# Kernel tuning notes

Measured on AMD Instinct MI355X. Metric: run time of the kernel, lower is better.

## Reference

```python
import jax, jax.numpy as jnp
import numpy as np

B, S, D, H = 8, 1300, 1080, 12
DK = D // H  # 90
FF = 3 * D   # 3240
EPS = 1e-5


def _layernorm(x, g, b):
    m = jnp.mean(x, axis=-1, keepdims=True)
    v = jnp.var(x, axis=-1, keepdims=True)
    return (x - m) * jax.lax.rsqrt(v + EPS) * g + b


def _rotate_half(x):
    x1, x2 = jnp.split(x, 2, axis=-1)
    return jnp.concatenate([-x2, x1], axis=-1)


def _rope(x, cos, sin):
    # x: [B,H,S,DK]; cos/sin: [S,DK] broadcast over batch/heads
    return x * cos + _rotate_half(x) * sin


def setup_inputs() -> dict:
    key = jax.random.key(0)
    ks = jax.random.split(key, 20)
    w = lambda k, sh: jax.random.normal(k, sh, dtype=jnp.float32) * 0.02
    inp = {
        'x': jax.random.normal(ks[0], (B, S, D), dtype=jnp.float32),
        'mask': jnp.tril(jnp.ones((S, S), dtype=jnp.int32))[None, None, :, :],
        'Wq': w(ks[1], (D, D)), 'bq': jnp.zeros((D,), jnp.float32),
        'Wk': w(ks[2], (D, D)), 'bk': jnp.zeros((D,), jnp.float32),
        'Wv': w(ks[3], (D, D)), 'bv': jnp.zeros((D,), jnp.float32),
        'Wo': w(ks[4], (D, D)), 'bo': jnp.zeros((D,), jnp.float32),
        'W1': w(ks[5], (D, FF)), 'b1': jnp.zeros((FF,), jnp.float32),
        'W2': w(ks[6], (FF, D)), 'b2': jnp.zeros((D,), jnp.float32),
        'W3': w(ks[7], (D, FF)), 'b3': jnp.zeros((FF,), jnp.float32),
        'ln1_g': jnp.ones((D,), jnp.float32), 'ln1_b': jnp.zeros((D,), jnp.float32),
        'ln2_g': jnp.ones((D,), jnp.float32), 'ln2_b': jnp.zeros((D,), jnp.float32),
    }
    # RoPE tables (buffers, not trainable)
    inv_freq = 1.0 / (10000.0 ** (jnp.arange(0, DK, 2, dtype=jnp.float32) / DK))
    t = jnp.arange(S, dtype=jnp.float32)
    freqs = t[:, None] * inv_freq[None, :]          # [S, DK/2]
    emb = jnp.concatenate([freqs, freqs], axis=-1)  # [S, DK]
    inp['rope_cos'] = jnp.cos(emb)
    inp['rope_sin'] = jnp.sin(emb)
    return inp


def reference(x, mask, Wq, bq, Wk, bk, Wv, bv, Wo, bo,
              W1, b1, W2, b2, W3, b3, ln1_g, ln1_b, ln2_g, ln2_b,
              rope_cos, rope_sin):
    # pre-norm attention block
    x2 = _layernorm(x, ln1_g, ln1_b)
    q = (x2 @ Wq + bq).reshape(B, S, H, DK).transpose(0, 2, 1, 3)  # [B,H,S,DK]
    k = (x2 @ Wk + bk).reshape(B, S, H, DK).transpose(0, 2, 1, 3)
    v = (x2 @ Wv + bv).reshape(B, S, H, DK).transpose(0, 2, 1, 3)
    q = _rope(q, rope_cos, rope_sin)
    k = _rope(k, rope_cos, rope_sin)
    scores = jnp.einsum('bhqd,bhkd->bhqk', q, k) / jnp.sqrt(jnp.float32(DK))
    scores = jnp.where(mask == 0, jnp.float32(-1e9), scores)
    p = jax.nn.softmax(scores, axis=-1)
    attn = jnp.einsum('bhqk,bhkd->bhqd', p, v)
    attn = attn.transpose(0, 2, 1, 3).reshape(B, S, D)
    x = x + (attn @ Wo + bo)
    # pre-norm SwiGLU FFN block
    x2 = _layernorm(x, ln2_g, ln2_b)
    h = jax.nn.silu(x2 @ W1 + b1) * (x2 @ W3 + b3)
    x = x + (h @ W2 + b2)
    return x
```

## Files before the change

### kernel.cpp

```cpp
#include <hip/hip_runtime.h>
#include <hip/hip_bf16.h>
#include <cstdint>
#include <cstddef>

#define B_  8
#define S_  1300
#define D_  1080
#define H_  12
#define DK_ 90
#define FF_ 3240
#define MROWS (B_*S_)
#define KP1 1088
#define KP2 3264
#define SP  1312
#define QKVN 3240
#define QSCALE 0.105409255338946f

typedef __hip_bfloat16 bf16;
typedef __bf16 bf16x8 __attribute__((ext_vector_type(8)));
typedef float  f32x4  __attribute__((ext_vector_type(4)));
typedef unsigned short u16x8 __attribute__((ext_vector_type(8)));

__device__ __forceinline__ void gload16(const void* g, void* l) {
    __builtin_amdgcn_global_load_lds((const __attribute__((address_space(1))) void*)g,
                                     (__attribute__((address_space(3))) void*)l, 16, 0, 0);
}
__device__ __forceinline__ unsigned short bf16bits(float f) {
    bf16 b = __float2bfloat16(f);
    return *(unsigned short*)&b;
}

__global__ __launch_bounds__(256) void zero_pads(bf16* __restrict__ buf)
{
    const int idx = blockIdx.x * 256 + threadIdx.x;
    if (idx >= MROWS * (KP1 - D_)) return;
    const int row = idx >> 3, col = D_ + (idx & 7);
    buf[(size_t)row * KP1 + col] = __float2bfloat16(0.f);
}

__global__ __launch_bounds__(256) void bcat(const float* __restrict__ bq,
    const float* __restrict__ bk, const float* __restrict__ bv,
    float* __restrict__ bqkv)
{
    const int i = blockIdx.x * 256 + threadIdx.x;
    if (i >= QKVN) return;
    bqkv[i] = (i < D_) ? bq[i] : (i < 2 * D_) ? bk[i - D_] : bv[i - 2 * D_];
}

__global__ __launch_bounds__(256) void castT(const float* __restrict__ W,
    bf16* __restrict__ WT, int K, int N, int KP)
{
    __shared__ unsigned short t[32][33];
    const int tx = threadIdx.x & 31, ty = threadIdx.x >> 5;
    const int k0 = blockIdx.x * 32, n0 = blockIdx.y * 32;
    #pragma unroll
    for (int i = 0; i < 4; ++i) {
        const int k = k0 + ty + 8 * i;
        const int n = n0 + tx;
        float v = (k < K && n < N) ? W[(size_t)k * N + n] : 0.f;
        t[ty + 8 * i][tx] = bf16bits(v);
    }
    __syncthreads();
    #pragma unroll
    for (int i = 0; i < 4; ++i) {
        const int n = n0 + ty + 8 * i;
        const int kk = k0 + tx;
        if (n < N && kk < KP) *(unsigned short*)&WT[(size_t)n * KP + kk] = t[tx][ty + 8 * i];
    }
}

__global__ __launch_bounds__(256) void ln_kernel(const float* __restrict__ x,
    const float* __restrict__ g, const float* __restrict__ b,
    bf16* __restrict__ y)
{
    __shared__ float xs[D_];
    __shared__ float red[8];
    const int row = blockIdx.x;
    const int tid = threadIdx.x;
    const float* xr = x + (size_t)row * D_;

    float s = 0.f, sq = 0.f;
    for (int d = tid; d < D_; d += 256) {
        float v = xr[d];
        xs[d] = v;
        s += v; sq += v * v;
    }
    #pragma unroll
    for (int off = 32; off > 0; off >>= 1) {
        s  += __shfl_down(s,  off, 64);
        sq += __shfl_down(sq, off, 64);
    }
    const int wave = tid >> 6, lane = tid & 63;
    if (lane == 0) { red[wave] = s; red[4 + wave] = sq; }
    __syncthreads();
    if (tid == 0) {
        float ts = 0.f, tq = 0.f;
        #pragma unroll
        for (int w = 0; w < 4; ++w) { ts += red[w]; tq += red[4 + w]; }
        red[0] = ts; red[4] = tq;
    }
    __syncthreads();
    const float mean = red[0] * (1.0f / D_);
    const float var  = red[4] * (1.0f / D_) - mean * mean;
    const float rstd = rsqrtf(var + 1e-5f);
    bf16* yr = y + (size_t)row * KP1;
    for (int d = tid; d < D_; d += 256)
        yr[d] = __float2bfloat16((xs[d] - mean) * rstd * g[d] + b[d]);
}

template<int MODE>
__global__ __launch_bounds__(256) void gemm_bf16(
    const bf16* __restrict__ A, const bf16* __restrict__ BT,
    const float* __restrict__ bias, const float* __restrict__ res,
    float* __restrict__ Cf, bf16* __restrict__ Cb,
    int M, int N, int KP, int LDC, int NP)
{
    __shared__ unsigned short As[128 * 32];
    __shared__ unsigned short Bs[128 * 32];

    const int tid = threadIdx.x;
    const int w = tid >> 6, l = tid & 63;
    const int m0 = blockIdx.y * 128, n0 = blockIdx.x * 128;

    const int rs = w * 16 + (l >> 2);
    const int kc = (l & 3) * 8;
    const int ar0 = min(m0 + rs,      M - 1);
    const int ar1 = min(m0 + rs + 64, M - 1);
    const int br0 = min(n0 + rs,      N - 1);
    const int br1 = min(n0 + rs + 64, N - 1);

    const int wm = (w >> 1) * 64, wn = (w & 1) * 64;
    const int lr = l & 15, kq = l >> 4;

    const unsigned short* aptr[4];
    const unsigned short* bptr[4];
    #pragma unroll
    for (int i = 0; i < 4; ++i) {
        aptr[i] = &As[(wm + i * 16 + lr) * 32 + kq * 8];
        bptr[i] = &Bs[(wn + i * 16 + lr) * 32 + kq * 8];
    }

    f32x4 acc[4][4] = {};

    const int nkt = KP >> 5;
    for (int kt = 0; kt < nkt; ++kt) {
        const int k0 = kt << 5;
        __syncthreads();
        gload16(A  + (size_t)ar0 * KP + k0 + kc, &As[w * 512]);
        gload16(A  + (size_t)ar1 * KP + k0 + kc, &As[2048 + w * 512]);
        gload16(BT + (size_t)br0 * KP + k0 + kc, &Bs[w * 512]);
        gload16(BT + (size_t)br1 * KP + k0 + kc, &Bs[2048 + w * 512]);
        __syncthreads();

        bf16x8 af[4], bv[4];
        #pragma unroll
        for (int i = 0; i < 4; ++i) af[i] = *(const bf16x8*)aptr[i];
        #pragma unroll
        for (int j = 0; j < 4; ++j) bv[j] = *(const bf16x8*)bptr[j];
        #pragma unroll
        for (int i = 0; i < 4; ++i)
            #pragma unroll
            for (int j = 0; j < 4; ++j)
                acc[i][j] = __builtin_amdgcn_mfma_f32_16x16x32_bf16(af[i], bv[j], acc[i][j], 0, 0, 0);
    }

    #pragma unroll
    for (int j = 0; j < 4; ++j) {
        const int n = n0 + wn + j * 16 + lr;
        if (n >= NP) continue;
        const bool real = (n < N);
        const float bn = real ? bias[n] : 0.f;
        #pragma unroll
        for (int i = 0; i < 4; ++i) {
            const int rowb = m0 + wm + i * 16 + kq * 4;
            #pragma unroll
            for (int r = 0; r < 4; ++r) {
                const int m = rowb + r;
                if (m < M) {
                    const size_t off = (size_t)m * LDC + n;
                    float val = acc[i][j][r] + bn;
                    if (MODE == 0) Cf[off] = val;
                    if (MODE == 1) Cf[off] = val + res[off];
                    if (MODE == 3) Cb[off] = real ? __float2bfloat16(val) : __float2bfloat16(0.f);
                    if (MODE == 2) {
                        if (real) {
                            const float prev = __bfloat162float(Cb[off]);
                            const float sig  = 1.0f / (1.0f + __expf(-prev));
                            Cb[off] = __float2bfloat16(prev * sig * val);
                        } else {
                            Cb[off] = __float2bfloat16(0.f);
                        }
                    }
                }
            }
        }
    }
}

__global__ __launch_bounds__(256) void rope_qk(const bf16* __restrict__ qkv,
    const float* __restrict__ cosb, const float* __restrict__ sinb,
    bf16* __restrict__ Qa, bf16* __restrict__ Ka)
{
    const int s = blockIdx.x;
    const int b = blockIdx.y;
    const int tid = threadIdx.x;

    if (s >= S_) {
        for (int idx = tid; idx < H_ * 96; idx += 256) {
            const int h = idx / 96, c = idx - (idx / 96) * 96;
            const size_t o = ((size_t)(b * H_ + h) * SP + s) * 96 + c;
            Qa[o] = __float2bfloat16(0.f);
            Ka[o] = __float2bfloat16(0.f);
        }
        return;
    }

    const bf16* row = qkv + (size_t)(b * S_ + s) * QKVN;

    for (int idx = tid; idx < H_ * 45; idx += 256) {
        const int h = idx / 45, d = idx - (idx / 45) * 45;
        const float c1 = cosb[s * DK_ + d],      s1 = sinb[s * DK_ + d];
        const float c2 = cosb[s * DK_ + d + 45], s2 = sinb[s * DK_ + d + 45];
        const size_t o = ((size_t)(b * H_ + h) * SP + s) * 96;
        const float q1 = __bfloat162float(row[h * DK_ + d]);
        const float q2 = __bfloat162float(row[h * DK_ + d + 45]);
        Qa[o + d]      = __float2bfloat16((q1 * c1 - q2 * s1) * QSCALE);
        Qa[o + d + 45] = __float2bfloat16((q2 * c2 + q1 * s2) * QSCALE);
        const float k1 = __bfloat162float(row[D_ + h * DK_ + d]);
        const float k2 = __bfloat162float(row[D_ + h * DK_ + d + 45]);
        Ka[o + d]      = __float2bfloat16(k1 * c1 - k2 * s1);
        Ka[o + d + 45] = __float2bfloat16(k2 * c2 + k1 * s2);
    }
    for (int idx = tid; idx < H_ * 6; idx += 256) {
        const int h = idx / 6, c = 90 + (idx - (idx / 6) * 6);
        const size_t o = ((size_t)(b * H_ + h) * SP + s) * 96 + c;
        Qa[o] = __float2bfloat16(0.f);
        Ka[o] = __float2bfloat16(0.f);
    }
}

__global__ __launch_bounds__(256) void vtrans(const bf16* __restrict__ qkv,
    bf16* __restrict__ Vt)
{
    __shared__ float T[96][33];
    const int k0 = blockIdx.x * 32;
    const int bh = blockIdx.y;
    const int b = bh / H_, h = bh % H_;
    const int tid = threadIdx.x;

    for (int idx = tid; idx < 32 * 90; idx += 256) {
        const int r = idx / 90, d = idx - (idx / 90) * 90;
        const int s = k0 + r;
        T[d][r] = (s < S_) ?
            __bfloat162float(qkv[(size_t)(b * S_ + s) * QKVN + 2 * D_ + h * DK_ + d]) : 0.f;
    }
    for (int idx = tid; idx < 32 * 6; idx += 256) {
        const int r = idx / 6, d = 90 + (idx - (idx / 6) * 6);
        T[d][r] = 0.f;
    }
    __syncthreads();
    for (int idx = tid; idx < 96 * 4; idx += 256) {
        const int d = idx >> 2, kk = (idx & 3) * 8;
        u16x8 v;
        #pragma unroll
        for (int i = 0; i < 8; ++i) v[i] = bf16bits(T[d][kk + i]);
        *(u16x8*)(Vt + ((size_t)bh * 96 + d) * SP + k0 + kk) = v;
    }
}

__global__ __launch_bounds__(256) void attn_mfma(const bf16* __restrict__ Qa,
    const bf16* __restrict__ Ka, const bf16* __restrict__ Vt,
    bf16* __restrict__ ab)
{
    __shared__ unsigned short Qs[64][104];
    __shared__ unsigned short Ks[32][104];
    __shared__ unsigned short Vs[96][40];
    __shared__ unsigned short Ps[4][16][40];

    const int tid = threadIdx.x;
    const int w = tid >> 6, l = tid & 63;
    const int lr = l & 15, kq = l >> 4;
    const int qblk = (int)gridDim.x - 1 - (int)blockIdx.x;
    const int q0 = qblk * 64;
    const int bh = blockIdx.y;
    const int b = bh / H_, h = bh % H_;

    const bf16* Qg = Qa + (size_t)bh * SP * 96;
    const bf16* Kg = Ka + (size_t)bh * SP * 96;
    const bf16* Vg = Vt + (size_t)bh * 96 * SP;

    for (int c = tid; c < 768; c += 256) {
        const int row = c / 12, cc = c - row * 12;
        const int rg = q0 + row;
        u16x8 v = (u16x8)0;
        if (rg < SP) v = *(const u16x8*)(Qg + (size_t)rg * 96 + cc * 8);
        *(u16x8*)&Qs[row][cc * 8] = v;
    }
    __syncthreads();

    bf16x8 Qf[3];
    #pragma unroll
    for (int kf = 0; kf < 3; ++kf)
        Qf[kf] = *(const bf16x8*)&Qs[w * 16 + lr][kf * 32 + kq * 8];

    const int qw0 = q0 + w * 16;
    const int myq = qw0 + lr;
    const int wlq = (qw0 < S_) ? min(qw0 + 15, S_ - 1) : -1;
    const int lastq = min(q0 + 63, S_ - 1);
    const int ntiles = lastq / 32 + 1;

    f32x4 Of[6] = {};
    float mrun = -1e30f, lrun = 0.f;

    for (int kt = 0; kt < ntiles; ++kt) {
        const int k0 = kt * 32;
        __syncthreads();
        for (int c = tid; c < 384; c += 256) {
            const int row = c / 12, cc = c - (c / 12) * 12;
            *(u16x8*)&Ks[row][cc * 8] = *(const u16x8*)(Kg + (size_t)(k0 + row) * 96 + cc * 8);
        }
        for (int c = tid; c < 384; c += 256) {
            const int d = c >> 2, kk = (c & 3) * 8;
            *(u16x8*)&Vs[d][kk] = *(const u16x8*)(Vg + (size_t)d * SP + k0 + kk);
        }
        __syncthreads();

        if (k0 > wlq) continue;

        f32x4 sg0 = {0.f, 0.f, 0.f, 0.f}, sg1 = {0.f, 0.f, 0.f, 0.f};
        #pragma unroll
        for (int kf = 0; kf < 3; ++kf) {
            bf16x8 k0f = *(const bf16x8*)&Ks[lr][kf * 32 + kq * 8];
            bf16x8 k1f = *(const bf16x8*)&Ks[16 + lr][kf * 32 + kq * 8];
            sg0 = __builtin_amdgcn_mfma_f32_16x16x32_bf16(k0f, Qf[kf], sg0, 0, 0, 0);
            sg1 = __builtin_amdgcn_mfma_f32_16x16x32_bf16(k1f, Qf[kf], sg1, 0, 0, 0);
        }

        float e[8];
        float msub = -1e30f;
        #pragma unroll
        for (int r = 0; r < 4; ++r) {
            const int ka = k0 + 4 * kq + r;
            const int kb = ka + 16;
            const float a = (ka <= myq && ka < S_) ? sg0[r] : -1e30f;
            const float c = (kb <= myq && kb < S_) ? sg1[r] : -1e30f;
            e[r] = a; e[4 + r] = c;
            msub = fmaxf(msub, fmaxf(a, c));
        }
        msub = fmaxf(msub, __shfl_xor(msub, 16, 64));
        msub = fmaxf(msub, __shfl_xor(msub, 32, 64));
        const float nm = fmaxf(mrun, msub);
        const float resc = __expf(mrun - nm);
        mrun = nm;
        float ls = 0.f;
        #pragma unroll
        for (int i = 0; i < 8; ++i) {
            const float ev = (e[i] > -1e29f) ? __expf(e[i] - nm) : 0.f;
            e[i] = ev; ls += ev;
        }
        ls += __shfl_xor(ls, 16, 64);
        ls += __shfl_xor(ls, 32, 64);
        lrun = lrun * resc + ls;

        ushort4 p0, p1;
        p0.x = bf16bits(e[0]); p0.y = bf16bits(e[1]); p0.z = bf16bits(e[2]); p0.w = bf16bits(e[3]);
        p1.x = bf16bits(e[4]); p1.y = bf16bits(e[5]); p1.z = bf16bits(e[6]); p1.w = bf16bits(e[7]);
        *(ushort4*)&Ps[w][lr][4 * kq]      = p0;
        *(ushort4*)&Ps[w][lr][16 + 4 * kq] = p1;

        float rf[4];
        #pragma unroll
        for (int r = 0; r < 4; ++r) rf[r] = __shfl(resc, 4 * kq + r, 16);
        #pragma unroll
        for (int c = 0; c < 6; ++c)
            #pragma unroll
            for (int r = 0; r < 4; ++r)
                Of[c][r] *= rf[r];

        bf16x8 Pf = *(const bf16x8*)&Ps[w][lr][kq * 8];
        #pragma unroll
        for (int c = 0; c < 6; ++c) {
            bf16x8 Vf = *(const bf16x8*)&Vs[16 * c + lr][kq * 8];
            Of[c] = __builtin_amdgcn_mfma_f32_16x16x32_bf16(Pf, Vf, Of[c], 0, 0, 0);
        }
    }

    const float invq = 1.0f / lrun;
    float inv[4];
    #pragma unroll
    for (int r = 0; r < 4; ++r) inv[r] = __shfl(invq, 4 * kq + r, 16);
    #pragma unroll
    for (int c = 0; c < 6; ++c) {
        const int dim = 16 * c + lr;
        if (dim >= DK_) continue;
        #pragma unroll
        for (int r = 0; r < 4; ++r) {
            const int qrow = qw0 + 4 * kq + r;
            if (qrow < S_)
                ab[(size_t)(b * S_ + qrow) * KP1 + h * DK_ + dim] =
                    __float2bfloat16(Of[c][r] * inv[r]);
        }
    }
}

extern "C" void kernel_launch(void* const* d_in, const int* in_sizes, int n_in,
                              void* d_out, int out_size, void* d_ws, size_t ws_size,
                              hipStream_t stream)
{
    const float* x    = (const float*)d_in[0];
    const float* Wq   = (const float*)d_in[2];
    const float* bq   = (const float*)d_in[3];
    const float* Wk   = (const float*)d_in[4];
    const float* bk   = (const float*)d_in[5];
    const float* Wv   = (const float*)d_in[6];
    const float* bv   = (const float*)d_in[7];
    const float* Wo   = (const float*)d_in[8];
    const float* bo   = (const float*)d_in[9];
    const float* W1   = (const float*)d_in[10];
    const float* b1   = (const float*)d_in[11];
    const float* W2   = (const float*)d_in[12];
    const float* b2   = (const float*)d_in[13];
    const float* W3   = (const float*)d_in[14];
    const float* b3   = (const float*)d_in[15];
    const float* ln1g = (const float*)d_in[16];
    const float* ln1b = (const float*)d_in[17];
    const float* ln2g = (const float*)d_in[18];
    const float* ln2b = (const float*)d_in[19];
    const float* rc   = (const float*)d_in[20];
    const float* rs   = (const float*)d_in[21];
    float* out = (float*)d_out;

    char* wsb = (char*)d_ws;
    size_t off = 0;
    auto nxt = [&](size_t bytes) -> char* {
        char* p = wsb + off; off += (bytes + 255) & ~(size_t)255; return p;
    };
    bf16*  x2   = (bf16*)nxt((size_t)MROWS * KP1 * 2);
    bf16*  qkv  = (bf16*)nxt((size_t)MROWS * KP2 * 2);
    float* x1f  = (float*)nxt((size_t)MROWS * D_ * 4);
    bf16*  ab   = (bf16*)nxt((size_t)MROWS * KP1 * 2);
    bf16*  WqkvT= (bf16*)nxt((size_t)QKVN * KP1 * 2);
    bf16*  WoT  = (bf16*)nxt((size_t)D_ * KP1 * 2);
    bf16*  W1T  = (bf16*)nxt((size_t)FF_ * KP1 * 2);
    bf16*  W3T  = (bf16*)nxt((size_t)FF_ * KP1 * 2);
    bf16*  W2T  = (bf16*)nxt((size_t)D_ * KP2 * 2);
    bf16*  Qa   = (bf16*)nxt((size_t)B_ * H_ * SP * 96 * 2);
    bf16*  Ka   = (bf16*)nxt((size_t)B_ * H_ * SP * 96 * 2);
    float* bqkv = (float*)nxt((size_t)QKVN * 4);
    bf16*  Vt   = (bf16*)x1f;
    float* x1   = x1f;
    bf16*  hb   = qkv;

    const dim3 blk(256);
    const dim3 gD(9, 82);
    const dim3 gF(26, 82);
    const int padN = MROWS * (KP1 - D_);

    zero_pads<<<(padN + 255) / 256, blk, 0, stream>>>(x2);
    zero_pads<<<(padN + 255) / 256, blk, 0, stream>>>(ab);
    bcat<<<(QKVN + 255) / 256, blk, 0, stream>>>(bq, bk, bv, bqkv);

    castT<<<dim3(34, 34),  blk, 0, stream>>>(Wq, WqkvT,                    D_, D_, KP1);
    castT<<<dim3(34, 34),  blk, 0, stream>>>(Wk, WqkvT + (size_t)D_ * KP1, D_, D_, KP1);
    castT<<<dim3(34, 34),  blk, 0, stream>>>(Wv, WqkvT + (size_t)2*D_*KP1, D_, D_, KP1);
    castT<<<dim3(34, 34),  blk, 0, stream>>>(Wo, WoT, D_, D_, KP1);
    castT<<<dim3(34, 102), blk, 0, stream>>>(W1, W1T, D_, FF_, KP1);
    castT<<<dim3(34, 102), blk, 0, stream>>>(W3, W3T, D_, FF_, KP1);
    castT<<<dim3(102, 34), blk, 0, stream>>>(W2, W2T, FF_, D_, KP2);

    ln_kernel<<<MROWS, blk, 0, stream>>>(x, ln1g, ln1b, x2);
    gemm_bf16<3><<<gF, blk, 0, stream>>>(x2, WqkvT, bqkv, nullptr, nullptr, qkv,
                                         MROWS, QKVN, KP1, QKVN, QKVN);
    rope_qk<<<dim3(SP, B_), blk, 0, stream>>>(qkv, rc, rs, Qa, Ka);
    vtrans<<<dim3(41, B_ * H_), blk, 0, stream>>>(qkv, Vt);
    attn_mfma<<<dim3(21, B_ * H_), blk, 0, stream>>>(Qa, Ka, Vt, ab);
    gemm_bf16<1><<<gD, blk, 0, stream>>>(ab, WoT, bo, x, x1, nullptr, MROWS, D_, KP1, D_, D_);
    ln_kernel<<<MROWS, blk, 0, stream>>>(x1, ln2g, ln2b, x2);
    gemm_bf16<3><<<gF, blk, 0, stream>>>(x2, W1T, b1, nullptr, nullptr, hb, MROWS, FF_, KP1, KP2, KP2);
    gemm_bf16<2><<<gF, blk, 0, stream>>>(x2, W3T, b3, nullptr, nullptr, hb, MROWS, FF_, KP1, KP2, KP2);
    gemm_bf16<1><<<gD, blk, 0, stream>>>(hb, W2T, b2, x1, out, nullptr, MROWS, D_, KP2, D_, D_);
}
```

Baseline: 1.144 ms.

## Triple-buffer GEMM LDS tiles with async prefetch and XOR-swizzled layout

Rewrites the bf16 GEMM main loop to use a three-slot LDS ring, issuing global-to-LDS loads two k-tiles ahead and waiting with vmcnt, so that only one barrier per iteration is needed. LDS reads use explicit ds_read_b128 on an XOR-swizzled layout to cut bank conflicts, with sched barriers to pin instruction order. It also sets a launch bound of 3 blocks per CU. The cost is more LDS per block (48KB), which may limit occupancy, and hand-written waitcnt logic that is fragile.

```diff
diff --git a/kernel.cpp b/kernel.cpp
--- a/kernel.cpp
+++ b/kernel.cpp
@@ -20,6 +20,7 @@
 typedef __bf16 bf16x8 __attribute__((ext_vector_type(8)));
 typedef float  f32x4  __attribute__((ext_vector_type(4)));
 typedef unsigned short u16x8 __attribute__((ext_vector_type(8)));
+typedef unsigned int   u32x4 __attribute__((ext_vector_type(4)));
 
 __device__ __forceinline__ void gload16(const void* g, void* l) {
     __builtin_amdgcn_global_load_lds((const __attribute__((address_space(1))) void*)g,
@@ -29,6 +30,15 @@
     bf16 b = __float2bfloat16(f);
     return *(unsigned short*)&b;
 }
+__device__ __forceinline__ bf16x8 dsr(unsigned byteaddr) {
+    union { u32x4 u; bf16x8 b; } c;
+    asm volatile("ds_read_b128 %0, %1" : "=&v"(c.u) : "v"(byteaddr));
+    return c.b;
+}
+
+#define BAR()   __builtin_amdgcn_s_barrier()
+#define LGKM0() asm volatile("s_waitcnt lgkmcnt(0)" ::: "memory")
+#define SCB()   __builtin_amdgcn_sched_barrier(0)
 
 __global__ __launch_bounds__(256) void zero_pads(bf16* __restrict__ buf)
 {
@@ -109,60 +119,80 @@
 }
 
 template<int MODE>
-__global__ __launch_bounds__(256) void gemm_bf16(
+__global__ __launch_bounds__(256, 3) void gemm_bf16(
     const bf16* __restrict__ A, const bf16* __restrict__ BT,
     const float* __restrict__ bias, const float* __restrict__ res,
     float* __restrict__ Cf, bf16* __restrict__ Cb,
     int M, int N, int KP, int LDC, int NP)
 {
-    __shared__ unsigned short As[128 * 32];
-    __shared__ unsigned short Bs[128 * 32];
+    __shared__ unsigned short lds[24576];
 
     const int tid = threadIdx.x;
     const int w = tid >> 6, l = tid & 63;
+    const int lr = l & 15, kq = l >> 4;
     const int m0 = blockIdx.y * 128, n0 = blockIdx.x * 128;
 
     const int rs = w * 16 + (l >> 2);
-    const int kc = (l & 3) * 8;
+    const int sx = ((l & 3) ^ ((l >> 3) & 3)) * 8;
     const int ar0 = min(m0 + rs,      M - 1);
     const int ar1 = min(m0 + rs + 64, M - 1);
     const int br0 = min(n0 + rs,      N - 1);
     const int br1 = min(n0 + rs + 64, N - 1);
+    const bf16* pa0 = A  + (size_t)ar0 * KP + sx;
+    const bf16* pa1 = A  + (size_t)ar1 * KP + sx;
+    const bf16* pb0 = BT + (size_t)br0 * KP + sx;
+    const bf16* pb1 = BT + (size_t)br1 * KP + sx;
 
     const int wm = (w >> 1) * 64, wn = (w & 1) * 64;
-    const int lr = l & 15, kq = l >> 4;
-
-    const unsigned short* aptr[4];
-    const unsigned short* bptr[4];
+
+    const unsigned ldsb = (unsigned)(size_t)(const __attribute__((address_space(3))) void*)&lds[0];
+    const unsigned co = (unsigned)((kq ^ ((lr >> 1) & 3)) << 4);
+    unsigned aoffB[4], boffB[4];
     #pragma unroll
     for (int i = 0; i < 4; ++i) {
-        aptr[i] = &As[(wm + i * 16 + lr) * 32 + kq * 8];
-        bptr[i] = &Bs[(wn + i * 16 + lr) * 32 + kq * 8];
+        aoffB[i] = ldsb + (unsigned)((wm + i * 16 + lr) * 64) + co;
+        boffB[i] = ldsb + 24576u + (unsigned)((wn + i * 16 + lr) * 64) + co;
     }
 
     f32x4 acc[4][4] = {};
-
     const int nkt = KP >> 5;
-    for (int kt = 0; kt < nkt; ++kt) {
-        const int k0 = kt << 5;
-        __syncthreads();
-        gload16(A  + (size_t)ar0 * KP + k0 + kc, &As[w * 512]);
-        gload16(A  + (size_t)ar1 * KP + k0 + kc, &As[2048 + w * 512]);
-        gload16(BT + (size_t)br0 * KP + k0 + kc, &Bs[w * 512]);
-        gload16(BT + (size_t)br1 * KP + k0 + kc, &Bs[2048 + w * 512]);
-        __syncthreads();
-
+
+#define STAGE(t, sl) do { \
+    gload16(pa0 + (size_t)(t) * 32, &lds[(sl) * 4096 + w * 512]); \
+    gload16(pa1 + (size_t)(t) * 32, &lds[(sl) * 4096 + 2048 + w * 512]); \
+    gload16(pb0 + (size_t)(t) * 32, &lds[12288 + (sl) * 4096 + w * 512]); \
+    gload16(pb1 + (size_t)(t) * 32, &lds[12288 + (sl) * 4096 + 2048 + w * 512]); \
+} while (0)
+
+    STAGE(0, 0);
+    STAGE(1, 1);
+
+    int sc_ = 0;
+    int ss_ = 2;
+    for (int t = 0; t < nkt; ++t) {
+        if (t + 1 < nkt) { asm volatile("s_waitcnt vmcnt(4)" ::: "memory"); }
+        else             { asm volatile("s_waitcnt vmcnt(0)" ::: "memory"); }
+        BAR(); SCB();
+        if (t + 2 < nkt) STAGE(t + 2, ss_);
+
+        const unsigned sb = (unsigned)(sc_ * 8192);
         bf16x8 af[4], bv[4];
         #pragma unroll
-        for (int i = 0; i < 4; ++i) af[i] = *(const bf16x8*)aptr[i];
-        #pragma unroll
-        for (int j = 0; j < 4; ++j) bv[j] = *(const bf16x8*)bptr[j];
+        for (int i = 0; i < 4; ++i) af[i] = dsr(aoffB[i] + sb);
+        #pragma unroll
+        for (int j = 0; j < 4; ++j) bv[j] = dsr(boffB[j] + sb);
+        LGKM0(); SCB();
         #pragma unroll
         for (int i = 0; i < 4; ++i)
             #pragma unroll
             for (int j = 0; j < 4; ++j)
                 acc[i][j] = __builtin_amdgcn_mfma_f32_16x16x32_bf16(af[i], bv[j], acc[i][j], 0, 0, 0);
-    }
+        SCB();
+
+        sc_ = (sc_ == 2) ? 0 : sc_ + 1;
+        ss_ = (ss_ == 2) ? 0 : ss_ + 1;
+    }
+#undef STAGE
 
     #pragma unroll
     for (int j = 0; j < 4; ++j) {
@@ -452,8 +482,8 @@
     bf16*  hb   = qkv;
 
     const dim3 blk(256);
+    const dim3 gF(26, 82);
     const dim3 gD(9, 82);
-    const dim3 gF(26, 82);
     const int padN = MROWS * (KP1 - D_);
 
     zero_pads<<<(padN + 255) / 256, blk, 0, stream>>>(x2);
```

Result: faster. 1.107 ms (-3.2%).
